# Kernel optimization log

Hardware: AMD Instinct MI355X
Metric: run time of the kernel (lower is better)

The kernel has to match this reference:

```python
import jax, jax.numpy as jnp
import numpy as np

GAMMA = 0.1    # gamma hard-coded in SoftDWT.forward
BIG = 1e10     # finite stand-in for +inf so softmin grads stay clean


def _soft_dtw(x, y, gamma):
    # x: (N,), y: (M,) univariate series; squared-Euclidean cost (tslearn default)
    N, M = x.shape[0], y.shape[0]
    D = (x[:, None] - y[None, :]) ** 2  # (N, M) pairwise cost
    i = jnp.arange(N)

    def step(carry, t):
        # carry holds R on anti-diagonals t-2 and t-1, indexed by row i (R[i, t-k-i])
        r2, r1 = carry
        j = t - i
        valid = (j >= 0) & (j < M)
        d = D[i, jnp.clip(j, 0, M - 1)]
        up = jnp.where(i > 0, jnp.roll(r1, 1), BIG)                   # R[i-1, j]
        left = jnp.where(j > 0, r1, BIG)                              # R[i, j-1]
        diag = jnp.where((i > 0) & (j > 0), jnp.roll(r2, 1), BIG)     # R[i-1, j-1]
        diag = jnp.where((i == 0) & (j == 0), 0.0, diag)              # virtual R[0,0] = 0
        v = jnp.stack([up, left, diag]) * (-1.0 / gamma)              # (3, N)
        smin = -gamma * jax.scipy.special.logsumexp(v, axis=0)        # stable soft-min
        r = jnp.where(valid, d + smin, BIG)
        return (r1, r), None

    init = (jnp.full((N,), BIG, dtype=x.dtype), jnp.full((N,), BIG, dtype=x.dtype))
    (_, r_last), _ = jax.lax.scan(step, init, jnp.arange(N + M - 1))
    return r_last[N - 1]  # R[N-1, M-1]


def setup_inputs() -> dict:
    key = jax.random.key(0)
    k1, k2 = jax.random.split(key)
    N = 4096
    return {
        "inputs": jax.random.normal(k1, (N,), dtype=jnp.float32),
        "targets": jax.random.normal(k2, (N,), dtype=jnp.float32),
    }


def reference(inputs, targets):
    # SoftDTWLossPyTorch(gamma=0.1) on batch of 1, then .abs().mean()
    sdtw = _soft_dtw(inputs, targets, GAMMA)
    return jnp.abs(sdtw)
```

## Files before the change

### kernel.cpp

```cpp
#include <hip/hip_runtime.h>
#include <math.h>


#define KS     14.426950408889634f
#define BIGP   1.4426950e+11f
#define NN     4096
#define POISON 0xAAAAAAAAu

__device__ __forceinline__ float dpp_shr1(float oldv, float src) {
    int o = __float_as_int(oldv), s = __float_as_int(src);
    return __int_as_float(__builtin_amdgcn_update_dpp(o, s, 0x138 , 0xF, 0xF, false));
}
__device__ __forceinline__ float rdlane(float v, int l) {
    return __int_as_float(__builtin_amdgcn_readlane(__float_as_int(v), l));
}
__device__ __forceinline__ float aload(const float* p) {
    unsigned u = __hip_atomic_load((const unsigned*)p, __ATOMIC_RELAXED, __HIP_MEMORY_SCOPE_AGENT);
    return __uint_as_float(u);
}
__device__ __forceinline__ void astore(float* p, float v) {
    __hip_atomic_store((unsigned*)p, __float_as_uint(v), __ATOMIC_RELAXED, __HIP_MEMORY_SCOPE_AGENT);
}

__global__ __launch_bounds__(64, 1)
void sdtw_band_kernel(const float* __restrict__ x, const float* __restrict__ y,
                      float* __restrict__ out, float* __restrict__ bnd) {
    __shared__ __align__(16) float sh[64 + NN + 128];
    const int band = blockIdx.x;
    const int lane = threadIdx.x;
    const float sqK = sqrtf(KS);

    sh[lane] = 0.0f;
    sh[64 + NN + lane] = 0.0f;
    sh[64 + NN + 64 + lane] = 0.0f;
    {
        const float4* y4 = (const float4*)y;
        float4* s4 = (float4*)(sh + 64);
        #pragma unroll 4
        for (int i = lane; i < NN / 4; i += 64) {
            float4 v = y4[i];
            v.x *= sqK; v.y *= sqK; v.z *= sqK; v.w *= sqK;
            s4[i] = v;
        }
    }
    __syncthreads();

    const float xs = x[band * 64 + lane] * sqK;
    float* bnd_my         = bnd + band * NN;
    const float* bnd_prev = bnd + (band - 1) * NN;
    const bool prod = (band < 63);
    const bool cons = (band > 0);

    float r1  = BIGP;
    float vdg = (band == 0 && lane == 0) ? 0.0f : BIGP;
    float rsave = 0.0f;

    float bsub = 0.0f, bnext = 0.0f;
    float yw[16], ywn[16];

    if (cons) bsub = aload(&bnd_prev[lane & 15]);
    #pragma unroll
    for (int k = 0; k < 16; ++k) yw[k] = sh[64 + k - lane];

    for (int c = 0; c < 260; ++c) {
        const int base = c * 16;
        if (cons && c <= 255) {
            int bail = 0;
            while ((__ballot(__float_as_uint(bsub) != POISON) & 0xFFFFull) != 0xFFFFull) {
                __builtin_amdgcn_s_sleep(1);
                bsub = aload(&bnd_prev[base + (lane & 15)]);
                if (++bail > (1 << 20)) break;
            }
        }
        if (cons && c < 255) bnext = aload(&bnd_prev[base + 16 + (lane & 15)]);
        {
            const int wb = 64 + base + 16 - lane;
            #pragma unroll
            for (int k = 0; k < 16; ++k) ywn[k] = sh[wb + k];
        }
        #pragma unroll
        for (int s = 0; s < 16; ++s) {
            float binj = cons ? rdlane(bsub, s) : BIGP;
            float vup  = dpp_shr1(binj, r1);
            float m    = fminf(fminf(vup, vdg), r1);
            float e1 = __builtin_amdgcn_exp2f(m - vup);
            float e3 = __builtin_amdgcn_exp2f(m - vdg);
            float e2 = __builtin_amdgcn_exp2f(m - r1);
            float lg = __builtin_amdgcn_logf((e1 + e3) + e2);
            float diff = xs - yw[s];
            float rn = fmaf(diff, diff, m) - lg;
            vdg = vup;
            r1  = rn;
            if (prod) {
                const int t = base + s;
                if (lane == 63 && t >= 63 && t <= 63 + NN - 1)
                    astore(&bnd_my[t - 63], rn);
            }
            if (s == 14 && c == 259) rsave = rn;
        }
        bsub = bnext;
        #pragma unroll
        for (int k = 0; k < 16; ++k) yw[k] = ywn[k];
    }

    if (band == 63 && lane == 63)
        out[0] = fabsf(rsave * (1.0f / KS));
}

extern "C" void kernel_launch(void* const* d_in, const int* in_sizes, int n_in,
                              void* d_out, int out_size, void* d_ws, size_t ws_size,
                              hipStream_t stream) {
    const float* x = (const float*)d_in[0];
    const float* y = (const float*)d_in[1];
    float* out = (float*)d_out;
    float* bnd = (float*)d_ws;
    sdtw_band_kernel<<<dim3(64), dim3(64), 0, stream>>>(x, y, out, bnd);
}
```

Measured before the change: 1.207 ms.

## Group eight bands per workgroup and pass boundaries through LDS

Restructures the wavefront pipeline so each workgroup runs eight 64-row bands as eight waves. Boundaries between waves inside a block go through shared memory with workgroup-scope atomics, and only block-to-block boundaries use global memory, with a two-chunk prefetch. The scaled y vector moves from LDS to a per-block global workspace, since LDS is now taken by the boundary buffers. The aim is lower producer-consumer latency between bands, at the cost of y reads coming from global/L2 and more waves sharing one CU.

Measured after the change: 1.378 ms. 14.2% more time.

```diff
diff --git a/kernel.cpp b/kernel.cpp
--- a/kernel.cpp
+++ b/kernel.cpp
@@ -6,6 +6,9 @@
 #define BIGP   1.4426950e+11f
 #define NN     4096
 #define POISON 0xAAAAAAAAu
+#define YPADF  64
+#define YPADB  192
+#define YTOT   (YPADF + NN + YPADB)
 
 __device__ __forceinline__ float dpp_shr1(float oldv, float src) {
     int o = __float_as_int(oldv), s = __float_as_int(src);
@@ -14,73 +17,96 @@
 __device__ __forceinline__ float rdlane(float v, int l) {
     return __int_as_float(__builtin_amdgcn_readlane(__float_as_int(v), l));
 }
-__device__ __forceinline__ float aload(const float* p) {
+__device__ __forceinline__ float aloadG(const float* p) {
     unsigned u = __hip_atomic_load((const unsigned*)p, __ATOMIC_RELAXED, __HIP_MEMORY_SCOPE_AGENT);
     return __uint_as_float(u);
 }
-__device__ __forceinline__ void astore(float* p, float v) {
+__device__ __forceinline__ void astoreG(float* p, float v) {
     __hip_atomic_store((unsigned*)p, __float_as_uint(v), __ATOMIC_RELAXED, __HIP_MEMORY_SCOPE_AGENT);
 }
+__device__ __forceinline__ float aloadL(const float* p) {
+    unsigned u = __hip_atomic_load((const unsigned*)p, __ATOMIC_RELAXED, __HIP_MEMORY_SCOPE_WORKGROUP);
+    return __uint_as_float(u);
+}
+__device__ __forceinline__ void astoreL(float* p, float v) {
+    __hip_atomic_store((unsigned*)p, __float_as_uint(v), __ATOMIC_RELAXED, __HIP_MEMORY_SCOPE_WORKGROUP);
+}
 
-__global__ __launch_bounds__(64, 1)
+__global__ __launch_bounds__(512, 1)
 void sdtw_band_kernel(const float* __restrict__ x, const float* __restrict__ y,
-                      float* __restrict__ out, float* __restrict__ bnd) {
-    __shared__ __align__(16) float sh[64 + NN + 128];
-    const int band = blockIdx.x;
-    const int lane = threadIdx.x;
+                      float* __restrict__ out, float* __restrict__ bndG,
+                      float* __restrict__ yws) {
+    __shared__ float shb[7][NN];
+    const int g    = blockIdx.x;
+    const int tid  = threadIdx.x;
+    const int w    = tid >> 6;
+    const int lane = tid & 63;
+    const int band = g * 8 + w;
     const float sqK = sqrtf(KS);
 
-    sh[lane] = 0.0f;
-    sh[64 + NN + lane] = 0.0f;
-    sh[64 + NN + 64 + lane] = 0.0f;
     {
-        const float4* y4 = (const float4*)y;
-        float4* s4 = (float4*)(sh + 64);
-        #pragma unroll 4
-        for (int i = lane; i < NN / 4; i += 64) {
-            float4 v = y4[i];
-            v.x *= sqK; v.y *= sqK; v.z *= sqK; v.w *= sqK;
-            s4[i] = v;
+        unsigned* shu = (unsigned*)&shb[0][0];
+        for (int i = tid; i < 7 * NN; i += 512) shu[i] = POISON;
+        float* yp0 = yws + g * YTOT;
+        for (int i = tid; i < YTOT; i += 512) {
+            int yi = i - YPADF;
+            yp0[i] = (yi >= 0 && yi < NN) ? y[yi] * sqK : 0.0f;
         }
     }
     __syncthreads();
 
+    const float* yp = yws + g * YTOT;
     const float xs = x[band * 64 + lane] * sqK;
-    float* bnd_my         = bnd + band * NN;
-    const float* bnd_prev = bnd + (band - 1) * NN;
-    const bool prod = (band < 63);
-    const bool cons = (band > 0);
+
+    const bool consL = (w > 0);
+    const bool consG = (w == 0 && g > 0);
+    const bool prodL = (w < 7);
+    const bool prodG = (w == 7 && g < 7);
+    float*       gout = bndG + g * NN;
+    const float* gin  = bndG + (g > 0 ? (g - 1) : 0) * NN;
+    const float* lin  = &shb[(w > 0 ? w - 1 : 0)][0];
+    float*       lout = &shb[(w < 7 ? w : 0)][0];
 
     float r1  = BIGP;
     float vdg = (band == 0 && lane == 0) ? 0.0f : BIGP;
     float rsave = 0.0f;
+    float yw[16], ywn[16];
+    float bcur = 0.0f, bnx = 0.0f;
 
-    float bsub = 0.0f, bnext = 0.0f;
-    float yw[16], ywn[16];
-
-    if (cons) bsub = aload(&bnd_prev[lane & 15]);
     #pragma unroll
-    for (int k = 0; k < 16; ++k) yw[k] = sh[64 + k - lane];
+    for (int k = 0; k < 16; ++k) yw[k] = yp[YPADF + k - lane];
+    if (consG) { bcur = aloadG(&gin[lane & 15]); bnx = aloadG(&gin[16 + (lane & 15)]); }
+    if (consL) { bcur = aloadL(&lin[lane & 15]); }
 
     for (int c = 0; c < 260; ++c) {
         const int base = c * 16;
-        if (cons && c <= 255) {
+        const int li   = base + (lane & 15);
+        if (consL && c <= 255) {
             int bail = 0;
-            while ((__ballot(__float_as_uint(bsub) != POISON) & 0xFFFFull) != 0xFFFFull) {
+            while ((__ballot(__float_as_uint(bcur) != POISON) & 0xFFFFull) != 0xFFFFull) {
                 __builtin_amdgcn_s_sleep(1);
-                bsub = aload(&bnd_prev[base + (lane & 15)]);
+                bcur = aloadL(&lin[li]);
+                if (++bail > (1 << 20)) break;
+            }
+            if (c < 255) bnx = aloadL(&lin[li + 16]);
+        } else if (consG && c <= 255) {
+            int bail = 0;
+            while ((__ballot(__float_as_uint(bcur) != POISON) & 0xFFFFull) != 0xFFFFull) {
+                __builtin_amdgcn_s_sleep(1);
+                bcur = aloadG(&gin[li]);
                 if (++bail > (1 << 20)) break;
             }
         }
-        if (cons && c < 255) bnext = aload(&bnd_prev[base + 16 + (lane & 15)]);
+        float btmp = 0.0f;
+        if (consG && c < 254) btmp = aloadG(&gin[li + 32]);
         {
-            const int wb = 64 + base + 16 - lane;
+            const float* yb = yp + YPADF + base + 16 - lane;
             #pragma unroll
-            for (int k = 0; k < 16; ++k) ywn[k] = sh[wb + k];
+            for (int k = 0; k < 16; ++k) ywn[k] = yb[k];
         }
         #pragma unroll
         for (int s = 0; s < 16; ++s) {
-            float binj = cons ? rdlane(bsub, s) : BIGP;
+            float binj = (consL || consG) ? rdlane(bcur, s) : BIGP;
             float vup  = dpp_shr1(binj, r1);
             float m    = fminf(fminf(vup, vdg), r1);
             float e1 = __builtin_amdgcn_exp2f(m - vup);
@@ -91,14 +117,15 @@
             float rn = fmaf(diff, diff, m) - lg;
             vdg = vup;
             r1  = rn;
-            if (prod) {
-                const int t = base + s;
-                if (lane == 63 && t >= 63 && t <= 63 + NN - 1)
-                    astore(&bnd_my[t - 63], rn);
+            const int t = base + s;
+            if (lane == 63 && t >= 63 && t <= 63 + NN - 1) {
+                if (prodL) astoreL(&lout[t - 63], rn);
+                if (prodG) astoreG(&gout[t - 63], rn);
             }
             if (s == 14 && c == 259) rsave = rn;
         }
-        bsub = bnext;
+        if (consG) { bcur = bnx; bnx = btmp; }
+        else if (consL) { bcur = bnx; }
         #pragma unroll
         for (int k = 0; k < 16; ++k) yw[k] = ywn[k];
     }
@@ -113,6 +140,7 @@
     const float* x = (const float*)d_in[0];
     const float* y = (const float*)d_in[1];
     float* out = (float*)d_out;
-    float* bnd = (float*)d_ws;
-    sdtw_band_kernel<<<dim3(64), dim3(64), 0, stream>>>(x, y, out, bnd);
+    float* bndG = (float*)d_ws;
+    float* yws  = (float*)d_ws + 8 * NN;
+    sdtw_band_kernel<<<dim3(8), dim3(512), 0, stream>>>(x, y, out, bndG, yws);
 }
```

## Group four bands per workgroup with LDS boundary handoff between waves

Applied to the files above, without the earlier changes.

Packs four row-bands into one 256-thread workgroup so three of every four band-to-band boundary handoffs go through shared memory instead of global atomics, leaving only 16 global handoffs. It also spins without sleep, polls for the next chunk before computing the current one, and batches the boundary stores at the end of each chunk. This is meant to cut the pipeline latency of the wavefront dependency chain across bands. The trade-off is that LDS busy-polling can contend between waves on the same CU, and batched stores could delay the consumer by one chunk.

Result: slower. 1.465 ms (+21.4%).

```diff
diff --git a/kernel.cpp b/kernel.cpp
--- a/kernel.cpp
+++ b/kernel.cpp
@@ -6,6 +6,11 @@
 #define BIGP   1.4426950e+11f
 #define NN     4096
 #define POISON 0xAAAAAAAAu
+#define YPADF  64
+#define YPADB  192
+#define YTOT   (YPADF + NN + YPADB)
+#define NWAVE  4
+#define NWG    16
 
 __device__ __forceinline__ float dpp_shr1(float oldv, float src) {
     int o = __float_as_int(oldv), s = __float_as_int(src);
@@ -14,73 +19,76 @@
 __device__ __forceinline__ float rdlane(float v, int l) {
     return __int_as_float(__builtin_amdgcn_readlane(__float_as_int(v), l));
 }
-__device__ __forceinline__ float aload(const float* p) {
-    unsigned u = __hip_atomic_load((const unsigned*)p, __ATOMIC_RELAXED, __HIP_MEMORY_SCOPE_AGENT);
-    return __uint_as_float(u);
-}
-__device__ __forceinline__ void astore(float* p, float v) {
-    __hip_atomic_store((unsigned*)p, __float_as_uint(v), __ATOMIC_RELAXED, __HIP_MEMORY_SCOPE_AGENT);
-}
 
-__global__ __launch_bounds__(64, 1)
-void sdtw_band_kernel(const float* __restrict__ x, const float* __restrict__ y,
-                      float* __restrict__ out, float* __restrict__ bnd) {
-    __shared__ __align__(16) float sh[64 + NN + 128];
-    const int band = blockIdx.x;
-    const int lane = threadIdx.x;
+__global__ __launch_bounds__(256, 1)
+void sdtw_kernel(const float* __restrict__ x, const float* __restrict__ y,
+                 float* __restrict__ out, float* __restrict__ bndG) {
+    __shared__ float    shy[YTOT];
+    __shared__ unsigned shb[NWAVE - 1][NN];
+    const int g = blockIdx.x, tid = threadIdx.x;
+    const int w = tid >> 6, lane = tid & 63;
+    const int band = g * NWAVE + w;
     const float sqK = sqrtf(KS);
 
-    sh[lane] = 0.0f;
-    sh[64 + NN + lane] = 0.0f;
-    sh[64 + NN + 64 + lane] = 0.0f;
-    {
-        const float4* y4 = (const float4*)y;
-        float4* s4 = (float4*)(sh + 64);
-        #pragma unroll 4
-        for (int i = lane; i < NN / 4; i += 64) {
-            float4 v = y4[i];
-            v.x *= sqK; v.y *= sqK; v.z *= sqK; v.w *= sqK;
-            s4[i] = v;
-        }
+    for (int i = tid; i < (NWAVE - 1) * NN; i += 256) (&shb[0][0])[i] = POISON;
+    for (int i = tid; i < YTOT; i += 256) {
+        int yi = i - YPADF;
+        shy[i] = (yi >= 0 && yi < NN) ? y[yi] * sqK : 0.0f;
     }
     __syncthreads();
 
     const float xs = x[band * 64 + lane] * sqK;
-    float* bnd_my         = bnd + band * NN;
-    const float* bnd_prev = bnd + (band - 1) * NN;
-    const bool prod = (band < 63);
-    const bool cons = (band > 0);
+    const bool consL = (w > 0), consG = (w == 0 && g > 0);
+    const bool prodL = (w < NWAVE - 1), prodG = (w == NWAVE - 1 && g < NWG - 1);
+    unsigned*                loutU = &shb[prodL ? w : 0][0];
+    const volatile unsigned* linU  = &shb[consL ? w - 1 : 0][0];
+    unsigned*       goutU = (unsigned*)(bndG + g * NN);
+    const unsigned* ginU  = (const unsigned*)(bndG + (g > 0 ? g - 1 : 0) * NN);
 
     float r1  = BIGP;
     float vdg = (band == 0 && lane == 0) ? 0.0f : BIGP;
     float rsave = 0.0f;
+    float yw[16], ywn[16];
+    float bcur = 0.0f, bnx = 0.0f;
+    const int myi = lane & 15;
 
-    float bsub = 0.0f, bnext = 0.0f;
-    float yw[16], ywn[16];
-
-    if (cons) bsub = aload(&bnd_prev[lane & 15]);
     #pragma unroll
-    for (int k = 0; k < 16; ++k) yw[k] = sh[64 + k - lane];
+    for (int k = 0; k < 16; ++k) yw[k] = shy[YPADF + k - lane];
+    if (consL) {
+        unsigned u; int bail = 0;
+        do { u = linU[myi]; } while (!__all(u != POISON) && ++bail < (1 << 22));
+        bcur = __uint_as_float(u);
+    } else if (consG) {
+        unsigned u; int bail = 0;
+        do { u = __hip_atomic_load(&ginU[myi], __ATOMIC_RELAXED, __HIP_MEMORY_SCOPE_AGENT); }
+        while (!__all(u != POISON) && ++bail < (1 << 22));
+        bcur = __uint_as_float(u);
+    }
 
     for (int c = 0; c < 260; ++c) {
         const int base = c * 16;
-        if (cons && c <= 255) {
-            int bail = 0;
-            while ((__ballot(__float_as_uint(bsub) != POISON) & 0xFFFFull) != 0xFFFFull) {
-                __builtin_amdgcn_s_sleep(1);
-                bsub = aload(&bnd_prev[base + (lane & 15)]);
-                if (++bail > (1 << 20)) break;
+        if (c + 1 <= 255) {
+            const int li = base + 16 + myi;
+            if (consL) {
+                unsigned u; int bail = 0;
+                do { u = linU[li]; } while (!__all(u != POISON) && ++bail < (1 << 22));
+                bnx = __uint_as_float(u);
+            } else if (consG) {
+                unsigned u; int bail = 0;
+                do { u = __hip_atomic_load(&ginU[li], __ATOMIC_RELAXED, __HIP_MEMORY_SCOPE_AGENT); }
+                while (!__all(u != POISON) && ++bail < (1 << 22));
+                bnx = __uint_as_float(u);
             }
         }
-        if (cons && c < 255) bnext = aload(&bnd_prev[base + 16 + (lane & 15)]);
         {
-            const int wb = 64 + base + 16 - lane;
+            const float* yb = shy + YPADF + base + 16 - lane;
             #pragma unroll
-            for (int k = 0; k < 16; ++k) ywn[k] = sh[wb + k];
+            for (int k = 0; k < 16; ++k) ywn[k] = yb[k];
         }
+        float rsv[16];
         #pragma unroll
         for (int s = 0; s < 16; ++s) {
-            float binj = cons ? rdlane(bsub, s) : BIGP;
+            float binj = (consL || consG) ? rdlane(bcur, s) : BIGP;
             float vup  = dpp_shr1(binj, r1);
             float m    = fminf(fminf(vup, vdg), r1);
             float e1 = __builtin_amdgcn_exp2f(m - vup);
@@ -89,16 +97,21 @@
             float lg = __builtin_amdgcn_logf((e1 + e3) + e2);
             float diff = xs - yw[s];
             float rn = fmaf(diff, diff, m) - lg;
-            vdg = vup;
-            r1  = rn;
-            if (prod) {
-                const int t = base + s;
-                if (lane == 63 && t >= 63 && t <= 63 + NN - 1)
-                    astore(&bnd_my[t - 63], rn);
+            vdg = vup; r1 = rn; rsv[s] = rn;
+        }
+        if (c == 259) rsave = rsv[14];
+        if (lane == 63 && (prodL || prodG)) {
+            #pragma unroll
+            for (int s = 0; s < 16; ++s) {
+                const int j = base + s - 63;
+                if (j >= 0 && j < NN) {
+                    if (prodL) *(volatile unsigned*)&loutU[j] = __float_as_uint(rsv[s]);
+                    else __hip_atomic_store(&goutU[j], __float_as_uint(rsv[s]),
+                                            __ATOMIC_RELAXED, __HIP_MEMORY_SCOPE_AGENT);
+                }
             }
-            if (s == 14 && c == 259) rsave = rn;
         }
-        bsub = bnext;
+        bcur = bnx;
         #pragma unroll
         for (int k = 0; k < 16; ++k) yw[k] = ywn[k];
     }
@@ -113,6 +126,6 @@
     const float* x = (const float*)d_in[0];
     const float* y = (const float*)d_in[1];
     float* out = (float*)d_out;
-    float* bnd = (float*)d_ws;
-    sdtw_band_kernel<<<dim3(64), dim3(64), 0, stream>>>(x, y, out, bnd);
+    float* bndG = (float*)d_ws;
+    sdtw_kernel<<<dim3(NWG), dim3(256), 0, stream>>>(x, y, out, bndG);
 }
```

## Carry soft-min state as exponent/mantissa pairs and defer the log

Applied to the files above, without the earlier changes.

Each cell's value is now kept as a (P, S) pair, so R = P - log2(S). That takes the per-cell log off the wavefront's serial dependency chain, and the log is computed only for the boundary lane that stores values for the next band. The hardware exp2 is replaced with a polynomial exp2 built from FMAs and ldexp. S is renormalized with frexp once per 16-step chunk so it does not overflow. The cost is more ALU instructions per cell and a different numerical path, which could shift accuracy.

New measurement: 1.647 ms. +36.5%, slower.

```diff
diff --git a/kernel.cpp b/kernel.cpp
--- a/kernel.cpp
+++ b/kernel.cpp
@@ -6,6 +6,9 @@
 #define BIGP   1.4426950e+11f
 #define NN     4096
 #define POISON 0xAAAAAAAAu
+#define YPADF  64
+#define YPADB  192
+#define YTOT   (YPADF + NN + YPADB)
 
 __device__ __forceinline__ float dpp_shr1(float oldv, float src) {
     int o = __float_as_int(oldv), s = __float_as_int(src);
@@ -21,90 +24,97 @@
 __device__ __forceinline__ void astore(float* p, float v) {
     __hip_atomic_store((unsigned*)p, __float_as_uint(v), __ATOMIC_RELAXED, __HIP_MEMORY_SCOPE_AGENT);
 }
+__device__ __forceinline__ float exp2p(float a) {
+    a = fmaxf(a, -150.0f);
+    float n = rintf(a);
+    float f = a - n;
+    float p = fmaf(f, 0.00133335581464f, 0.00961812910763f);
+    p = fmaf(f, p, 0.0555041086648f);
+    p = fmaf(f, p, 0.240226506959f);
+    p = fmaf(f, p, 0.693147180560f);
+    p = fmaf(f, p, 1.0f);
+    return ldexpf(p, (int)n);
+}
 
 __global__ __launch_bounds__(64, 1)
-void sdtw_band_kernel(const float* __restrict__ x, const float* __restrict__ y,
-                      float* __restrict__ out, float* __restrict__ bnd) {
-    __shared__ __align__(16) float sh[64 + NN + 128];
+void sdtw_kernel(const float* __restrict__ x, const float* __restrict__ y,
+                 float* __restrict__ out, float* __restrict__ bnd) {
+    __shared__ float shy[YTOT];
     const int band = blockIdx.x;
     const int lane = threadIdx.x;
     const float sqK = sqrtf(KS);
 
-    sh[lane] = 0.0f;
-    sh[64 + NN + lane] = 0.0f;
-    sh[64 + NN + 64 + lane] = 0.0f;
-    {
-        const float4* y4 = (const float4*)y;
-        float4* s4 = (float4*)(sh + 64);
-        #pragma unroll 4
-        for (int i = lane; i < NN / 4; i += 64) {
-            float4 v = y4[i];
-            v.x *= sqK; v.y *= sqK; v.z *= sqK; v.w *= sqK;
-            s4[i] = v;
-        }
+    for (int i = lane; i < YTOT; i += 64) {
+        int yi = i - YPADF;
+        shy[i] = (yi >= 0 && yi < NN) ? y[yi] * sqK : 0.0f;
     }
     __syncthreads();
 
     const float xs = x[band * 64 + lane] * sqK;
     float* bnd_my         = bnd + band * NN;
-    const float* bnd_prev = bnd + (band - 1) * NN;
+    const float* bnd_prev = bnd + (band > 0 ? band - 1 : 0) * NN;
     const bool prod = (band < 63);
     const bool cons = (band > 0);
 
-    float r1  = BIGP;
-    float vdg = (band == 0 && lane == 0) ? 0.0f : BIGP;
-    float rsave = 0.0f;
+    float Pp = BIGP, Sp = 1.0f;
+    float Pd = (band == 0 && lane == 0) ? 0.0f : BIGP, Sd = 1.0f;
+    float rsP = 0.0f, rsS = 1.0f;
+    float yw[16], ywn[16];
+    float bcur = 0.0f, bnext = 0.0f;
 
-    float bsub = 0.0f, bnext = 0.0f;
-    float yw[16], ywn[16];
-
-    if (cons) bsub = aload(&bnd_prev[lane & 15]);
     #pragma unroll
-    for (int k = 0; k < 16; ++k) yw[k] = sh[64 + k - lane];
+    for (int k = 0; k < 16; ++k) yw[k] = shy[YPADF + k - lane];
+    if (cons) bcur = aload(&bnd_prev[lane & 15]);
 
     for (int c = 0; c < 260; ++c) {
         const int base = c * 16;
         if (cons && c <= 255) {
             int bail = 0;
-            while ((__ballot(__float_as_uint(bsub) != POISON) & 0xFFFFull) != 0xFFFFull) {
+            while ((__ballot(__float_as_uint(bcur) != POISON) & 0xFFFFull) != 0xFFFFull) {
                 __builtin_amdgcn_s_sleep(1);
-                bsub = aload(&bnd_prev[base + (lane & 15)]);
+                bcur = aload(&bnd_prev[base + (lane & 15)]);
                 if (++bail > (1 << 20)) break;
             }
         }
         if (cons && c < 255) bnext = aload(&bnd_prev[base + 16 + (lane & 15)]);
         {
-            const int wb = 64 + base + 16 - lane;
+            const float* yb = shy + YPADF + base + 16 - lane;
             #pragma unroll
-            for (int k = 0; k < 16; ++k) ywn[k] = sh[wb + k];
+            for (int k = 0; k < 16; ++k) ywn[k] = yb[k];
         }
         #pragma unroll
         for (int s = 0; s < 16; ++s) {
-            float binj = cons ? rdlane(bsub, s) : BIGP;
-            float vup  = dpp_shr1(binj, r1);
-            float m    = fminf(fminf(vup, vdg), r1);
-            float e1 = __builtin_amdgcn_exp2f(m - vup);
-            float e3 = __builtin_amdgcn_exp2f(m - vdg);
-            float e2 = __builtin_amdgcn_exp2f(m - r1);
-            float lg = __builtin_amdgcn_logf((e1 + e3) + e2);
+            float binj = cons ? rdlane(bcur, s) : BIGP;
+            float PU = dpp_shr1(binj, Pp);
+            float SU = dpp_shr1(1.0f, Sp);
+            float mu = fminf(fminf(PU, Pd), Pp);
+            float eU = exp2p(mu - PU);
+            float eD = exp2p(mu - Pd);
+            float eL = exp2p(mu - Pp);
+            float Sn = fmaf(eU, SU, fmaf(eD, Sd, eL * Sp));
             float diff = xs - yw[s];
-            float rn = fmaf(diff, diff, m) - lg;
-            vdg = vup;
-            r1  = rn;
+            float Pn = fmaf(diff, diff, mu);
             if (prod) {
+                float rh = Pn - __builtin_amdgcn_logf(Sn);
                 const int t = base + s;
                 if (lane == 63 && t >= 63 && t <= 63 + NN - 1)
-                    astore(&bnd_my[t - 63], rn);
+                    astore(&bnd_my[t - 63], rh);
             }
-            if (s == 14 && c == 259) rsave = rn;
+            Pd = PU; Sd = SU; Pp = Pn; Sp = Sn;
+            if (c == 259 && s == 14) { rsP = Pn; rsS = Sn; }
         }
-        bsub = bnext;
+        {
+            int e1, e2;
+            float m1 = frexpf(Sp, &e1); Sp = m1; Pp -= (float)e1;
+            float m2 = frexpf(Sd, &e2); Sd = m2; Pd -= (float)e2;
+        }
+        bcur = bnext;
         #pragma unroll
         for (int k = 0; k < 16; ++k) yw[k] = ywn[k];
     }
 
     if (band == 63 && lane == 63)
-        out[0] = fabsf(rsave * (1.0f / KS));
+        out[0] = fabsf((rsP - __builtin_amdgcn_logf(rsS)) * (1.0f / KS));
 }
 
 extern "C" void kernel_launch(void* const* d_in, const int* in_sizes, int n_in,
@@ -114,5 +124,5 @@
     const float* y = (const float*)d_in[1];
     float* out = (float*)d_out;
     float* bnd = (float*)d_ws;
-    sdtw_band_kernel<<<dim3(64), dim3(64), 0, stream>>>(x, y, out, bnd);
+    sdtw_kernel<<<dim3(64), dim3(64), 0, stream>>>(x, y, out, bnd);
 }
```
